# Optimization experiments

Hardware: AMD Instinct MI355X
Metric: run time of the kernel (lower is better)

## Reference

```python
import jax, jax.numpy as jnp
import numpy as np

B, N, D_IN, D, E, MAXD = 16, 512, 256, 64, 32, 50
LN_EPS = 1e-5

def setup_inputs() -> dict:
    key = jax.random.key(0)
    ks = jax.random.split(key, 24)
    s = lambda fan: 1.0 / np.sqrt(fan)
    inp = {
        'x': jax.random.normal(ks[0], (B, N, D_IN), jnp.float32),
        'price_rising_ranks': jax.random.randint(ks[1], (B, N), 0, N, jnp.int64),
        'Wp': jax.random.normal(ks[2], (D_IN, D), jnp.float32) * s(D_IN),
        'bp': jnp.zeros((D,), jnp.float32),
        'Wq': jax.random.normal(ks[3], (D, D), jnp.float32) * s(D),
        'bq': jnp.zeros((D,), jnp.float32),
        'Wk': jax.random.normal(ks[4], (D, D), jnp.float32) * s(D),
        'bk': jnp.zeros((D,), jnp.float32),
        'Wv': jax.random.normal(ks[5], (D, D), jnp.float32) * s(D),
        'bv': jnp.zeros((D,), jnp.float32),
        'Eemb': jax.random.normal(ks[6], (MAXD + 1, E), jnp.float32),
        'Wr1': jax.random.normal(ks[7], (E, 16), jnp.float32) * s(E),
        'br1': jnp.zeros((16,), jnp.float32),
        'Wr2': jax.random.normal(ks[8], (16, 1), jnp.float32) * s(16),
        'Wf1': jax.random.normal(ks[9], (D, 2 * D), jnp.float32) * s(D),
        'bf1': jnp.zeros((2 * D,), jnp.float32),
        'Wf2': jax.random.normal(ks[10], (2 * D, D), jnp.float32) * s(2 * D),
        'bf2': jnp.zeros((D,), jnp.float32),
        'ln_g': jnp.ones((D,), jnp.float32),
        'ln_b': jnp.zeros((D,), jnp.float32),
        'Ws1': jax.random.normal(ks[11], (D, 32), jnp.float32) * s(D),
        'bs1': jnp.zeros((32,), jnp.float32),
        'Ws2': jax.random.normal(ks[12], (32, 1), jnp.float32) * s(32),
        'bs2': jnp.zeros((1,), jnp.float32),
    }
    return inp

def reference(x, price_rising_ranks, Wp, bp, Wq, bq, Wk, bk, Wv, bv,
              Eemb, Wr1, br1, Wr2, Wf1, bf1, Wf2, bf2, ln_g, ln_b,
              Ws1, bs1, Ws2, bs2):
    xp = x @ Wp + bp                                  # (B,N,D)
    q = xp @ Wq + bq
    k = xp @ Wk + bk
    v = xp @ Wv + bv
    scores = jnp.einsum('bnd,bmd->bnm', q, k) / jnp.sqrt(jnp.float32(D))
    # rank-distance pairwise bias
    r = price_rising_ranks
    dists = jnp.clip(jnp.abs(r[:, :, None] - r[:, None, :]), 0, MAXD)  # (B,N,N) int
    emb = Eemb[dists]                                 # (B,N,N,E)
    w = jax.nn.relu(emb @ Wr1 + br1) @ Wr2            # (B,N,N,1)
    rel = jax.nn.sigmoid(w[..., 0])                   # (B,N,N)
    scores = scores * rel
    attn = jax.nn.softmax(scores, axis=-1)
    ao = jnp.einsum('bnm,bmd->bnd', attn, v)
    # feed forward + layernorm
    h = jax.nn.relu(ao @ Wf1 + bf1) @ Wf2 + bf2
    mu = jnp.mean(h, axis=-1, keepdims=True)
    var = jnp.mean((h - mu) ** 2, axis=-1, keepdims=True)
    hn = (h - mu) / jnp.sqrt(var + LN_EPS) * ln_g + ln_b
    # score projection
    out = jax.nn.relu(hn @ Ws1 + bs1) @ Ws2 + bs2     # (B,N,1)
    return jax.nn.sigmoid(out[..., 0])                # (B,N)
```

## Files before the change

kernel.cpp:

```cpp
#include <hip/hip_runtime.h>

using f32x4 = __attribute__((ext_vector_type(4))) float;
using s16x8 = __attribute__((ext_vector_type(8))) short;

static __device__ __forceinline__ unsigned short f2bf(float f){
  union { float f; unsigned int i; } c; c.f = f;
  return (unsigned short)((c.i + 0x7FFFu + ((c.i >> 16) & 1u)) >> 16);
}
static __device__ __forceinline__ s16x8 ld8(const unsigned short* p){
  return *(const s16x8*)p;
}
static __device__ __forceinline__ s16x8 cvt8(const float* p){
  const float4* q = (const float4*)p;
  float4 a = q[0], b = q[1];
  s16x8 r;
  r[0]=(short)f2bf(a.x); r[1]=(short)f2bf(a.y); r[2]=(short)f2bf(a.z); r[3]=(short)f2bf(a.w);
  r[4]=(short)f2bf(b.x); r[5]=(short)f2bf(b.y); r[6]=(short)f2bf(b.z); r[7]=(short)f2bf(b.w);
  return r;
}
static __device__ __forceinline__ f32x4 mfma16(s16x8 a, s16x8 b, f32x4 c){
  return __builtin_amdgcn_mfma_f32_16x16x32_bf16(a, b, c, 0, 0, 0);
}

__global__ __launch_bounds__(128) void k_proj(const float* __restrict__ x,
    const float* __restrict__ Wp, const float* __restrict__ bp,
    const float* __restrict__ Wq, const float* __restrict__ bq,
    const float* __restrict__ Wk, const float* __restrict__ bk,
    const float* __restrict__ Wv, const float* __restrict__ bv,
    const float* __restrict__ Ee, const float* __restrict__ Wr1,
    const float* __restrict__ br1, const float* __restrict__ Wr2,
    unsigned short* __restrict__ q, unsigned short* __restrict__ kk,
    unsigned short* __restrict__ vt, float* __restrict__ rel_t)
{
  __shared__ __align__(16) unsigned short WpT[64*264];
  __shared__ __align__(16) unsigned short Wt3[3][64*72];
  __shared__ __align__(16) unsigned short xs[2][16*72];

  int t = threadIdx.x;
  for (int i = t; i < 256*64; i += 128){
    int k = i >> 6, n = i & 63;
    WpT[n*264 + k] = f2bf(Wp[i]);
  }
  for (int i = t; i < 64*64; i += 128){
    int k2 = i >> 6, n = i & 63;
    Wt3[0][n*72 + k2] = f2bf(Wq[i]);
    Wt3[1][n*72 + k2] = f2bf(Wk[i]);
    Wt3[2][n*72 + k2] = f2bf(Wv[i]);
  }
  if (blockIdx.x == 0 && t < 51){
    float e[32];
    for (int j = 0; j < 32; ++j) e[j] = Ee[t*32 + j];
    float w = 0.f;
    for (int h = 0; h < 16; ++h){
      float s = br1[h];
      for (int j = 0; j < 32; ++j) s += e[j] * Wr1[j*16 + h];
      w += fmaxf(s, 0.f) * Wr2[h];
    }
    rel_t[t] = 1.f / (1.f + __expf(-w));
  }
  __syncthreads();

  int lane = t & 63, wave = t >> 6, colL = lane & 15, quad = lane >> 4;
  int row0 = blockIdx.x*32 + wave*16;

  const float* xr = x + (row0 + colL)*256;
  f32x4 acc[4] = {};
  for (int kc = 0; kc < 256; kc += 32){
    s16x8 a = cvt8(xr + kc + quad*8);
#pragma unroll
    for (int nt = 0; nt < 4; ++nt)
      acc[nt] = mfma16(a, ld8(&WpT[(nt*16+colL)*264 + kc + quad*8]), acc[nt]);
  }
  unsigned short* xw = xs[wave];
#pragma unroll
  for (int nt = 0; nt < 4; ++nt){
    int col = nt*16 + colL;
    float bb = bp[col];
#pragma unroll
    for (int i = 0; i < 4; ++i)
      xw[(quad*4+i)*72 + col] = f2bf(acc[nt][i] + bb);
  }
  s16x8 a0 = ld8(&xw[colL*72 +  0 + quad*8]);
  s16x8 a1 = ld8(&xw[colL*72 + 32 + quad*8]);

#pragma unroll
  for (int w = 0; w < 3; ++w){
    const float* bias = w==0 ? bq : (w==1 ? bk : bv);
    f32x4 c[4] = {};
#pragma unroll
    for (int nt = 0; nt < 4; ++nt){
      c[nt] = mfma16(a0, ld8(&Wt3[w][(nt*16+colL)*72 +  0 + quad*8]), c[nt]);
      c[nt] = mfma16(a1, ld8(&Wt3[w][(nt*16+colL)*72 + 32 + quad*8]), c[nt]);
    }
#pragma unroll
    for (int nt = 0; nt < 4; ++nt){
      int col = nt*16 + colL;
      float bb = bias[col];
#pragma unroll
      for (int i = 0; i < 4; ++i){
        int row = row0 + quad*4 + i;
        float v = c[nt][i] + bb;
        if (w == 0)      q [row*64 + col] = f2bf(v);
        else if (w == 1) kk[row*64 + col] = f2bf(v);
        else             vt[(row>>9)*32768 + col*512 + (row & 511)] = f2bf(v);
      }
    }
  }
}

__global__ __launch_bounds__(256) void k_attn(const unsigned short* __restrict__ q,
    const unsigned short* __restrict__ kmat, const unsigned short* __restrict__ vt,
    const int* __restrict__ ranks, const float* __restrict__ rel_t,
    unsigned short* __restrict__ ao)
{
  int b = blockIdx.y, qt = blockIdx.x;
  int t = threadIdx.x, lane = t & 63, wave = t >> 6;
  int colL = lane & 15, quad = lane >> 4;

  __shared__ int r_s[512];
  __shared__ float rt_s[64];
  __shared__ __align__(16) unsigned short P[4][16*136];
  __shared__ float Opart[4][16*66];
  __shared__ float pmax_s[4][16], psum_s[4][16];

  for (int i = t; i < 512; i += 256) r_s[i] = ranks[b*512 + i];
  if (t < 64) rt_s[t] = (t < 51) ? rel_t[t] : 0.f;
  __syncthreads();

  int qrow0 = qt*16;
  const unsigned short* qp = q    + b*32768;
  const unsigned short* kp = kmat + b*32768;
  const unsigned short* vp = vt   + b*32768;

  s16x8 aq0 = ld8(qp + (qrow0+colL)*64 +  0 + quad*8);
  s16x8 aq1 = ld8(qp + (qrow0+colL)*64 + 32 + quad*8);

  int key0 = wave*128;
  f32x4 S[8];
#pragma unroll
  for (int mt = 0; mt < 8; ++mt){
    int key = key0 + mt*16 + colL;
    f32x4 c = {};
    c = mfma16(aq0, ld8(kp + key*64 +  0 + quad*8), c);
    c = mfma16(aq1, ld8(kp + key*64 + 32 + quad*8), c);
    S[mt] = c;
  }

  int rq[4];
#pragma unroll
  for (int i = 0; i < 4; ++i) rq[i] = r_s[qrow0 + quad*4 + i];

  float rmax[4] = {-1e30f,-1e30f,-1e30f,-1e30f};
#pragma unroll
  for (int mt = 0; mt < 8; ++mt){
    int rm = r_s[key0 + mt*16 + colL];
#pragma unroll
    for (int i = 0; i < 4; ++i){
      int dd = rq[i] - rm; dd = dd < 0 ? -dd : dd; dd = dd > 50 ? 50 : dd;
      float s = S[mt][i] * 0.125f * rt_s[dd];
      S[mt][i] = s;
      rmax[i] = fmaxf(rmax[i], s);
    }
  }
#pragma unroll
  for (int i = 0; i < 4; ++i){
    rmax[i] = fmaxf(rmax[i], __shfl_xor(rmax[i], 1));
    rmax[i] = fmaxf(rmax[i], __shfl_xor(rmax[i], 2));
    rmax[i] = fmaxf(rmax[i], __shfl_xor(rmax[i], 4));
    rmax[i] = fmaxf(rmax[i], __shfl_xor(rmax[i], 8));
  }
  if (colL == 0){
#pragma unroll
    for (int i = 0; i < 4; ++i) pmax_s[wave][quad*4 + i] = rmax[i];
  }
  __syncthreads();
  float gmax[4];
#pragma unroll
  for (int i = 0; i < 4; ++i){
    int r = quad*4 + i;
    gmax[i] = fmaxf(fmaxf(pmax_s[0][r], pmax_s[1][r]), fmaxf(pmax_s[2][r], pmax_s[3][r]));
  }
  float rsum[4] = {0.f,0.f,0.f,0.f};
#pragma unroll
  for (int mt = 0; mt < 8; ++mt){
#pragma unroll
    for (int i = 0; i < 4; ++i){
      float p = __expf(S[mt][i] - gmax[i]);
      S[mt][i] = p;
      rsum[i] += p;
    }
  }
#pragma unroll
  for (int i = 0; i < 4; ++i){
    rsum[i] += __shfl_xor(rsum[i], 1);
    rsum[i] += __shfl_xor(rsum[i], 2);
    rsum[i] += __shfl_xor(rsum[i], 4);
    rsum[i] += __shfl_xor(rsum[i], 8);
  }
  if (colL == 0){
#pragma unroll
    for (int i = 0; i < 4; ++i) psum_s[wave][quad*4 + i] = rsum[i];
  }
  __syncthreads();
  float inv[4];
#pragma unroll
  for (int i = 0; i < 4; ++i){
    int r = quad*4 + i;
    inv[i] = 1.f / (psum_s[0][r] + psum_s[1][r] + psum_s[2][r] + psum_s[3][r]);
  }
  unsigned short* Pw = P[wave];
#pragma unroll
  for (int mt = 0; mt < 8; ++mt){
#pragma unroll
    for (int i = 0; i < 4; ++i)
      Pw[(quad*4+i)*136 + mt*16 + colL] = f2bf(S[mt][i] * inv[i]);
  }
  f32x4 O[4] = {};
#pragma unroll
  for (int mc = 0; mc < 128; mc += 32){
    s16x8 ap = ld8(&Pw[colL*136 + mc + quad*8]);
#pragma unroll
    for (int dt = 0; dt < 4; ++dt)
      O[dt] = mfma16(ap, ld8(vp + (dt*16+colL)*512 + key0 + mc + quad*8), O[dt]);
  }
  float* Ow = Opart[wave];
#pragma unroll
  for (int dt = 0; dt < 4; ++dt)
#pragma unroll
    for (int i = 0; i < 4; ++i)
      Ow[(quad*4+i)*66 + dt*16 + colL] = O[dt][i];
  __syncthreads();
  for (int e = t; e < 1024; e += 256){
    int row = e >> 6, col = e & 63;
    float s = Opart[0][row*66+col] + Opart[1][row*66+col]
            + Opart[2][row*66+col] + Opart[3][row*66+col];
    ao[(b*512 + qrow0 + row)*64 + col] = f2bf(s);
  }
}

__global__ __launch_bounds__(128) void k_ffn(const unsigned short* __restrict__ ao,
    const float* __restrict__ Wf1, const float* __restrict__ bf1,
    const float* __restrict__ Wf2, const float* __restrict__ bf2,
    const float* __restrict__ lng, const float* __restrict__ lnb,
    const float* __restrict__ Ws1, const float* __restrict__ bs1,
    const float* __restrict__ Ws2, const float* __restrict__ bs2,
    float* __restrict__ out)
{
  __shared__ __align__(16) unsigned short Wf1t[128*72];
  __shared__ __align__(16) unsigned short Wf2t[64*136];
  __shared__ __align__(16) unsigned short Ws1t[32*72];
  __shared__ __align__(16) unsigned short hbuf[2][16*136];
  __shared__ float cb[384];

  int t = threadIdx.x;
  for (int i = t; i < 64*128; i += 128){ int d = i>>7, j = i&127; Wf1t[j*72 + d] = f2bf(Wf1[i]); }
  for (int i = t; i < 128*64; i += 128){ int kx = i>>6, n = i&63; Wf2t[n*136 + kx] = f2bf(Wf2[i]); }
  for (int i = t; i < 64*32;  i += 128){ int d = i>>5, c = i&31; Ws1t[c*72 + d] = f2bf(Ws1[i]); }
  if (t < 128) cb[t] = bf1[t];
  if (t < 64){ cb[128+t] = bf2[t]; cb[192+t] = lng[t]; cb[256+t] = lnb[t]; }
  if (t < 32){ cb[320+t] = bs1[t]; cb[352+t] = Ws2[t]; }
  __syncthreads();

  int lane = t & 63, wave = t >> 6, colL = lane & 15, quad = lane >> 4;
  int row0 = blockIdx.x*32 + wave*16;
  unsigned short* hw = hbuf[wave];

  f32x4 a1[8] = {};
#pragma unroll
  for (int kc = 0; kc < 64; kc += 32){
    s16x8 a = ld8(ao + (row0+colL)*64 + kc + quad*8);
#pragma unroll
    for (int nt = 0; nt < 8; ++nt)
      a1[nt] = mfma16(a, ld8(&Wf1t[(nt*16+colL)*72 + kc + quad*8]), a1[nt]);
  }
#pragma unroll
  for (int nt = 0; nt < 8; ++nt){
    int col = nt*16 + colL;
    float bb = cb[col];
#pragma unroll
    for (int i = 0; i < 4; ++i)
      hw[(quad*4+i)*136 + col] = f2bf(fmaxf(a1[nt][i] + bb, 0.f));
  }
  f32x4 a2[4] = {};
#pragma unroll
  for (int kc = 0; kc < 128; kc += 32){
    s16x8 a = ld8(&hw[colL*136 + kc + quad*8]);
#pragma unroll
    for (int nt = 0; nt < 4; ++nt)
      a2[nt] = mfma16(a, ld8(&Wf2t[(nt*16+colL)*136 + kc + quad*8]), a2[nt]);
  }
  float vals[4][4];
#pragma unroll
  for (int nt = 0; nt < 4; ++nt){
    float bb = cb[128 + nt*16 + colL];
#pragma unroll
    for (int i = 0; i < 4; ++i) vals[i][nt] = a2[nt][i] + bb;
  }
  float hnv[4][4];
#pragma unroll
  for (int i = 0; i < 4; ++i){
    float s = vals[i][0]+vals[i][1]+vals[i][2]+vals[i][3];
    s += __shfl_xor(s,1); s += __shfl_xor(s,2); s += __shfl_xor(s,4); s += __shfl_xor(s,8);
    float mu = s * (1.f/64.f);
    float d0=vals[i][0]-mu, d1=vals[i][1]-mu, d2=vals[i][2]-mu, d3=vals[i][3]-mu;
    float s2 = d0*d0 + d1*d1 + d2*d2 + d3*d3;
    s2 += __shfl_xor(s2,1); s2 += __shfl_xor(s2,2); s2 += __shfl_xor(s2,4); s2 += __shfl_xor(s2,8);
    float invs = rsqrtf(s2*(1.f/64.f) + 1e-5f);
#pragma unroll
    for (int nt = 0; nt < 4; ++nt){
      int col = nt*16 + colL;
      hnv[i][nt] = (vals[i][nt]-mu)*invs*cb[192+col] + cb[256+col];
    }
  }
#pragma unroll
  for (int i = 0; i < 4; ++i)
#pragma unroll
    for (int nt = 0; nt < 4; ++nt)
      hw[(quad*4+i)*72 + nt*16 + colL] = f2bf(hnv[i][nt]);

  f32x4 a3[2] = {};
#pragma unroll
  for (int kc = 0; kc < 64; kc += 32){
    s16x8 a = ld8(&hw[colL*72 + kc + quad*8]);
#pragma unroll
    for (int nt = 0; nt < 2; ++nt)
      a3[nt] = mfma16(a, ld8(&Ws1t[(nt*16+colL)*72 + kc + quad*8]), a3[nt]);
  }
  float bs2f = bs2[0];
#pragma unroll
  for (int i = 0; i < 4; ++i){
    float p = 0.f;
#pragma unroll
    for (int nt = 0; nt < 2; ++nt){
      int col = nt*16 + colL;
      p += fmaxf(a3[nt][i] + cb[320+col], 0.f) * cb[352+col];
    }
    p += __shfl_xor(p,1); p += __shfl_xor(p,2); p += __shfl_xor(p,4); p += __shfl_xor(p,8);
    if (colL == 0){
      float z = p + bs2f;
      out[row0 + quad*4 + i] = 1.f / (1.f + __expf(-z));
    }
  }
}

extern "C" void kernel_launch(void* const* d_in, const int* in_sizes, int n_in,
                              void* d_out, int out_size, void* d_ws, size_t ws_size,
                              hipStream_t stream)
{
  const float* x    = (const float*)d_in[0];
  const int*   rank = (const int*)d_in[1];
  const float* Wp   = (const float*)d_in[2];
  const float* bp   = (const float*)d_in[3];
  const float* Wq   = (const float*)d_in[4];
  const float* bq   = (const float*)d_in[5];
  const float* Wk   = (const float*)d_in[6];
  const float* bk   = (const float*)d_in[7];
  const float* Wv   = (const float*)d_in[8];
  const float* bv   = (const float*)d_in[9];
  const float* Ee   = (const float*)d_in[10];
  const float* Wr1  = (const float*)d_in[11];
  const float* br1  = (const float*)d_in[12];
  const float* Wr2  = (const float*)d_in[13];
  const float* Wf1  = (const float*)d_in[14];
  const float* bf1  = (const float*)d_in[15];
  const float* Wf2  = (const float*)d_in[16];
  const float* bf2  = (const float*)d_in[17];
  const float* lng  = (const float*)d_in[18];
  const float* lnb  = (const float*)d_in[19];
  const float* Ws1  = (const float*)d_in[20];
  const float* bs1  = (const float*)d_in[21];
  const float* Ws2  = (const float*)d_in[22];
  const float* bs2  = (const float*)d_in[23];
  float* out = (float*)d_out;

  char* ws = (char*)d_ws;
  float*          rel_t = (float*)(ws + 0);
  unsigned short* q     = (unsigned short*)(ws + 256);
  unsigned short* kk    = (unsigned short*)(ws + 256 + 1*1048576);
  unsigned short* vt    = (unsigned short*)(ws + 256 + 2*1048576);
  unsigned short* ao    = (unsigned short*)(ws + 256 + 3*1048576);

  k_proj<<<dim3(256), dim3(128), 0, stream>>>(x, Wp, bp, Wq, bq, Wk, bk, Wv, bv,
                                              Ee, Wr1, br1, Wr2, q, kk, vt, rel_t);
  k_attn<<<dim3(32, 16), dim3(256), 0, stream>>>(q, kk, vt, rank, rel_t, ao);
  k_ffn<<<dim3(256), dim3(128), 0, stream>>>(ao, Wf1, bf1, Wf2, bf2, lng, lnb,
                                             Ws1, bs1, Ws2, bs2, out);
}
```

Before: 146.4 us.

## Fuse projection, attention and FFN into one cooperative kernel with grid sync

Replaces the three separate launches (projection, attention, FFN) with a single cooperative kernel of 256 blocks x 512 threads. Phases are separated by a grid-wide sync, and attention output stays in LDS so the FFN runs without a global round trip for ao. The rel-bias table and FFN weight staging are built per block in parallel with the projection waves. The aim is to remove launch gaps and the ao write/read. In exchange it relies on cooperative launch residency (the old three-kernel path is kept as a fallback) and pays the cost of a grid barrier and redundant per-block weight conversion.

Result: slower. 277.7 us (+89.7%).

```diff
diff --git a/kernel.cpp b/kernel.cpp
--- a/kernel.cpp
+++ b/kernel.cpp
@@ -1,4 +1,7 @@
 #include <hip/hip_runtime.h>
+#include <hip/hip_cooperative_groups.h>
+
+namespace cg = cooperative_groups;
 
 using f32x4 = __attribute__((ext_vector_type(4))) float;
 using s16x8 = __attribute__((ext_vector_type(8))) short;
@@ -20,6 +23,325 @@
 }
 static __device__ __forceinline__ f32x4 mfma16(s16x8 a, s16x8 b, f32x4 c){
   return __builtin_amdgcn_mfma_f32_16x16x32_bf16(a, b, c, 0, 0, 0);
+}
+
+struct Params {
+  const float *x; const int *ranks;
+  const float *Wp, *bp, *Wq, *bq, *Wk, *bk, *Wv, *bv;
+  const float *Ee, *Wr1, *br1, *Wr2;
+  const float *Wf1, *bf1, *Wf2, *bf2, *lng, *lnb, *Ws1, *bs1, *Ws2, *bs2;
+  unsigned short *qg, *kg, *vg;
+  float *out;
+};
+
+__global__ __launch_bounds__(512, 2) void k_fused(Params P)
+{
+  __shared__ __align__(16) char sm[118528];
+  int*   r_s    = (int*)  sm;
+  float* rt_s   = (float*)(sm + 2048);
+  float* pmax_s = (float*)(sm + 2304);
+  float* psum_s = (float*)(sm + 2816);
+  unsigned short* aoS  = (unsigned short*)(sm + 3328);
+  unsigned short* Wf1t = (unsigned short*)(sm + 7936);
+  unsigned short* Wf2t = (unsigned short*)(sm + 26368);
+  unsigned short* Ws1t = (unsigned short*)(sm + 43776);
+  float* cb            = (float*)(sm + 48384);
+  char* scr = sm + 49920;
+  unsigned short* WpT  = (unsigned short*)scr;
+  unsigned short* Wt3  = (unsigned short*)(scr + 33792);
+  unsigned short* xs   = (unsigned short*)(scr + 61440);
+  unsigned short* Pbuf = (unsigned short*)scr;
+  float*          Opart= (float*)(scr + 34816);
+  unsigned short* hbuf = (unsigned short*)scr;
+
+  int t = threadIdx.x, bid = blockIdx.x;
+  int lane = t & 63, wave = t >> 6, colL = lane & 15, quad = lane >> 4;
+
+  for (int i = t; i < 256*64; i += 512){ int k = i >> 6, n = i & 63; WpT[n*264 + k] = f2bf(P.Wp[i]); }
+  for (int i = t; i < 64*64; i += 512){
+    int k2 = i >> 6, n = i & 63;
+    Wt3[       n*72 + k2] = f2bf(P.Wq[i]);
+    Wt3[4608 + n*72 + k2] = f2bf(P.Wk[i]);
+    Wt3[9216 + n*72 + k2] = f2bf(P.Wv[i]);
+  }
+  r_s[t] = P.ranks[(bid >> 4)*512 + t];
+  __syncthreads();
+
+  if (wave < 2){
+    int row0 = bid*32 + wave*16;
+    const float* xr = P.x + (row0 + colL)*256;
+    f32x4 acc[4] = {};
+    for (int kc = 0; kc < 256; kc += 32){
+      s16x8 a = cvt8(xr + kc + quad*8);
+#pragma unroll
+      for (int nt = 0; nt < 4; ++nt)
+        acc[nt] = mfma16(a, ld8(&WpT[(nt*16+colL)*264 + kc + quad*8]), acc[nt]);
+    }
+    unsigned short* xw = xs + wave*(16*72);
+#pragma unroll
+    for (int nt = 0; nt < 4; ++nt){
+      int col = nt*16 + colL;
+      float bb = P.bp[col];
+#pragma unroll
+      for (int i = 0; i < 4; ++i)
+        xw[(quad*4+i)*72 + col] = f2bf(acc[nt][i] + bb);
+    }
+    s16x8 a0 = ld8(&xw[colL*72 +  0 + quad*8]);
+    s16x8 a1 = ld8(&xw[colL*72 + 32 + quad*8]);
+#pragma unroll
+    for (int w = 0; w < 3; ++w){
+      const float* bias = w==0 ? P.bq : (w==1 ? P.bk : P.bv);
+      const unsigned short* Wt = Wt3 + w*4608;
+      f32x4 c[4] = {};
+#pragma unroll
+      for (int nt = 0; nt < 4; ++nt){
+        c[nt] = mfma16(a0, ld8(&Wt[(nt*16+colL)*72 +  0 + quad*8]), c[nt]);
+        c[nt] = mfma16(a1, ld8(&Wt[(nt*16+colL)*72 + 32 + quad*8]), c[nt]);
+      }
+#pragma unroll
+      for (int nt = 0; nt < 4; ++nt){
+        int col = nt*16 + colL;
+        float bb = bias[col];
+#pragma unroll
+        for (int i = 0; i < 4; ++i){
+          int row = row0 + quad*4 + i;
+          float v = c[nt][i] + bb;
+          if (w == 0)      P.qg[row*64 + col] = f2bf(v);
+          else if (w == 1) P.kg[row*64 + col] = f2bf(v);
+          else             P.vg[(row>>9)*32768 + col*512 + (row & 511)] = f2bf(v);
+        }
+      }
+    }
+  } else if (wave == 7){
+    int dd = t - 448;
+    if (dd < 51){
+      float e[32];
+#pragma unroll
+      for (int j = 0; j < 32; ++j) e[j] = P.Ee[dd*32 + j];
+      float w = 0.f;
+      for (int h = 0; h < 16; ++h){
+        float s = P.br1[h];
+#pragma unroll
+        for (int j = 0; j < 32; ++j) s += e[j] * P.Wr1[j*16 + h];
+        w += fmaxf(s, 0.f) * P.Wr2[h];
+      }
+      rt_s[dd] = 1.f / (1.f + __expf(-w));
+    } else {
+      rt_s[dd] = 0.f;
+    }
+  } else {
+    int u = t - 128;
+    for (int i = u; i < 64*128; i += 320){ int d = i>>7, j = i&127; Wf1t[j*72 + d] = f2bf(P.Wf1[i]); }
+    for (int i = u; i < 128*64; i += 320){ int kx = i>>6, n = i&63; Wf2t[n*136 + kx] = f2bf(P.Wf2[i]); }
+    for (int i = u; i < 64*32;  i += 320){ int d = i>>5, c = i&31; Ws1t[c*72 + d] = f2bf(P.Ws1[i]); }
+    if (u < 128) cb[u] = P.bf1[u];
+    if (u < 64){ cb[128+u] = P.bf2[u]; cb[192+u] = P.lng[u]; cb[256+u] = P.lnb[u]; }
+    if (u < 32){ cb[320+u] = P.bs1[u]; cb[352+u] = P.Ws2[u]; }
+  }
+
+  __threadfence();
+  cg::this_grid().sync();
+  __threadfence();
+
+  int group = wave >> 2, kw = wave & 3;
+  {
+    int l = bid*2 + group;
+    int b = l >> 5, qt = l & 31;
+    int qrow0 = qt*16;
+    const unsigned short* qp = P.qg + b*32768;
+    const unsigned short* kp = P.kg + b*32768;
+    const unsigned short* vp = P.vg + b*32768;
+
+    s16x8 aq0 = ld8(qp + (qrow0+colL)*64 +  0 + quad*8);
+    s16x8 aq1 = ld8(qp + (qrow0+colL)*64 + 32 + quad*8);
+
+    int key0 = kw*128;
+    f32x4 Sv[8];
+#pragma unroll
+    for (int mt = 0; mt < 8; ++mt){
+      int key = key0 + mt*16 + colL;
+      f32x4 c = {};
+      c = mfma16(aq0, ld8(kp + key*64 +  0 + quad*8), c);
+      c = mfma16(aq1, ld8(kp + key*64 + 32 + quad*8), c);
+      Sv[mt] = c;
+    }
+
+    int rq[4];
+#pragma unroll
+    for (int i = 0; i < 4; ++i) rq[i] = r_s[qrow0 + quad*4 + i];
+
+    float rmax[4] = {-1e30f,-1e30f,-1e30f,-1e30f};
+#pragma unroll
+    for (int mt = 0; mt < 8; ++mt){
+      int rm = r_s[key0 + mt*16 + colL];
+#pragma unroll
+      for (int i = 0; i < 4; ++i){
+        int dd = rq[i] - rm; dd = dd < 0 ? -dd : dd; dd = dd > 50 ? 50 : dd;
+        float s = Sv[mt][i] * 0.125f * rt_s[dd];
+        Sv[mt][i] = s;
+        rmax[i] = fmaxf(rmax[i], s);
+      }
+    }
+#pragma unroll
+    for (int i = 0; i < 4; ++i){
+      rmax[i] = fmaxf(rmax[i], __shfl_xor(rmax[i], 1));
+      rmax[i] = fmaxf(rmax[i], __shfl_xor(rmax[i], 2));
+      rmax[i] = fmaxf(rmax[i], __shfl_xor(rmax[i], 4));
+      rmax[i] = fmaxf(rmax[i], __shfl_xor(rmax[i], 8));
+    }
+    if (colL == 0){
+#pragma unroll
+      for (int i = 0; i < 4; ++i) pmax_s[wave*16 + quad*4 + i] = rmax[i];
+    }
+    __syncthreads();
+    float gmax[4];
+#pragma unroll
+    for (int i = 0; i < 4; ++i){
+      int r = (group*4)*16 + quad*4 + i;
+      gmax[i] = fmaxf(fmaxf(pmax_s[r], pmax_s[r+16]), fmaxf(pmax_s[r+32], pmax_s[r+48]));
+    }
+    float rsum[4] = {0.f,0.f,0.f,0.f};
+#pragma unroll
+    for (int mt = 0; mt < 8; ++mt){
+#pragma unroll
+      for (int i = 0; i < 4; ++i){
+        float p = __expf(Sv[mt][i] - gmax[i]);
+        Sv[mt][i] = p;
+        rsum[i] += p;
+      }
+    }
+#pragma unroll
+    for (int i = 0; i < 4; ++i){
+      rsum[i] += __shfl_xor(rsum[i], 1);
+      rsum[i] += __shfl_xor(rsum[i], 2);
+      rsum[i] += __shfl_xor(rsum[i], 4);
+      rsum[i] += __shfl_xor(rsum[i], 8);
+    }
+    if (colL == 0){
+#pragma unroll
+      for (int i = 0; i < 4; ++i) psum_s[wave*16 + quad*4 + i] = rsum[i];
+    }
+    __syncthreads();
+    float inv[4];
+#pragma unroll
+    for (int i = 0; i < 4; ++i){
+      int r = (group*4)*16 + quad*4 + i;
+      inv[i] = 1.f / (psum_s[r] + psum_s[r+16] + psum_s[r+32] + psum_s[r+48]);
+    }
+    unsigned short* Pw = Pbuf + wave*(16*136);
+#pragma unroll
+    for (int mt = 0; mt < 8; ++mt){
+#pragma unroll
+      for (int i = 0; i < 4; ++i)
+        Pw[(quad*4+i)*136 + mt*16 + colL] = f2bf(Sv[mt][i] * inv[i]);
+    }
+    f32x4 O[4] = {};
+#pragma unroll
+    for (int mc = 0; mc < 128; mc += 32){
+      s16x8 ap = ld8(&Pw[colL*136 + mc + quad*8]);
+#pragma unroll
+      for (int dt = 0; dt < 4; ++dt)
+        O[dt] = mfma16(ap, ld8(vp + (dt*16+colL)*512 + key0 + mc + quad*8), O[dt]);
+    }
+    float* Ow = Opart + wave*(16*66);
+#pragma unroll
+    for (int dt = 0; dt < 4; ++dt)
+#pragma unroll
+      for (int i = 0; i < 4; ++i)
+        Ow[(quad*4+i)*66 + dt*16 + colL] = O[dt][i];
+    __syncthreads();
+    int tg = t & 255;
+    const float* Og = Opart + (group*4)*(16*66);
+    for (int e = tg; e < 1024; e += 256){
+      int row = e >> 6, col = e & 63;
+      float s = Og[row*66+col] + Og[1056 + row*66+col]
+              + Og[2112 + row*66+col] + Og[3168 + row*66+col];
+      aoS[(group*16 + row)*72 + col] = f2bf(s);
+    }
+  }
+  __syncthreads();
+
+  if (wave < 2){
+    unsigned short* hw = hbuf + wave*(16*136);
+    int row0 = bid*32 + wave*16;
+
+    f32x4 a1[8] = {};
+#pragma unroll
+    for (int kc = 0; kc < 64; kc += 32){
+      s16x8 a = ld8(&aoS[(wave*16 + colL)*72 + kc + quad*8]);
+#pragma unroll
+      for (int nt = 0; nt < 8; ++nt)
+        a1[nt] = mfma16(a, ld8(&Wf1t[(nt*16+colL)*72 + kc + quad*8]), a1[nt]);
+    }
+#pragma unroll
+    for (int nt = 0; nt < 8; ++nt){
+      int col = nt*16 + colL;
+      float bb = cb[col];
+#pragma unroll
+      for (int i = 0; i < 4; ++i)
+        hw[(quad*4+i)*136 + col] = f2bf(fmaxf(a1[nt][i] + bb, 0.f));
+    }
+    f32x4 a2[4] = {};
+#pragma unroll
+    for (int kc = 0; kc < 128; kc += 32){
+      s16x8 a = ld8(&hw[colL*136 + kc + quad*8]);
+#pragma unroll
+      for (int nt = 0; nt < 4; ++nt)
+        a2[nt] = mfma16(a, ld8(&Wf2t[(nt*16+colL)*136 + kc + quad*8]), a2[nt]);
+    }
+    float vals[4][4];
+#pragma unroll
+    for (int nt = 0; nt < 4; ++nt){
+      float bb = cb[128 + nt*16 + colL];
+#pragma unroll
+      for (int i = 0; i < 4; ++i) vals[i][nt] = a2[nt][i] + bb;
+    }
+    float hnv[4][4];
+#pragma unroll
+    for (int i = 0; i < 4; ++i){
+      float s = vals[i][0]+vals[i][1]+vals[i][2]+vals[i][3];
+      s += __shfl_xor(s,1); s += __shfl_xor(s,2); s += __shfl_xor(s,4); s += __shfl_xor(s,8);
+      float mu = s * (1.f/64.f);
+      float d0=vals[i][0]-mu, d1=vals[i][1]-mu, d2=vals[i][2]-mu, d3=vals[i][3]-mu;
+      float s2 = d0*d0 + d1*d1 + d2*d2 + d3*d3;
+      s2 += __shfl_xor(s2,1); s2 += __shfl_xor(s2,2); s2 += __shfl_xor(s2,4); s2 += __shfl_xor(s2,8);
+      float invs = rsqrtf(s2*(1.f/64.f) + 1e-5f);
+#pragma unroll
+      for (int nt = 0; nt < 4; ++nt){
+        int col = nt*16 + colL;
+        hnv[i][nt] = (vals[i][nt]-mu)*invs*cb[192+col] + cb[256+col];
+      }
+    }
+#pragma unroll
+    for (int i = 0; i < 4; ++i)
+#pragma unroll
+      for (int nt = 0; nt < 4; ++nt)
+        hw[(quad*4+i)*72 + nt*16 + colL] = f2bf(hnv[i][nt]);
+
+    f32x4 a3[2] = {};
+#pragma unroll
+    for (int kc = 0; kc < 64; kc += 32){
+      s16x8 a = ld8(&hw[colL*72 + kc + quad*8]);
+#pragma unroll
+      for (int nt = 0; nt < 2; ++nt)
+        a3[nt] = mfma16(a, ld8(&Ws1t[(nt*16+colL)*72 + kc + quad*8]), a3[nt]);
+    }
+    float bs2f = P.bs2[0];
+#pragma unroll
+    for (int i = 0; i < 4; ++i){
+      float p = 0.f;
+#pragma unroll
+      for (int nt = 0; nt < 2; ++nt){
+        int col = nt*16 + colL;
+        p += fmaxf(a3[nt][i] + cb[320+col], 0.f) * cb[352+col];
+      }
+      p += __shfl_xor(p,1); p += __shfl_xor(p,2); p += __shfl_xor(p,4); p += __shfl_xor(p,8);
+      if (colL == 0){
+        float z = p + bs2f;
+        P.out[row0 + quad*4 + i] = 1.f / (1.f + __expf(-z));
+      }
+    }
+  }
 }
 
 __global__ __launch_bounds__(128) void k_proj(const float* __restrict__ x,
@@ -119,7 +441,7 @@
 
   __shared__ int r_s[512];
   __shared__ float rt_s[64];
-  __shared__ __align__(16) unsigned short P[4][16*136];
+  __shared__ __align__(16) unsigned short Pl[4][16*136];
   __shared__ float Opart[4][16*66];
   __shared__ float pmax_s[4][16], psum_s[4][16];
 
@@ -208,7 +530,7 @@
     int r = quad*4 + i;
     inv[i] = 1.f / (psum_s[0][r] + psum_s[1][r] + psum_s[2][r] + psum_s[3][r]);
   }
-  unsigned short* Pw = P[wave];
+  unsigned short* Pw = Pl[wave];
 #pragma unroll
   for (int mt = 0; mt < 8; ++mt){
 #pragma unroll
@@ -380,9 +702,18 @@
   unsigned short* vt    = (unsigned short*)(ws + 256 + 2*1048576);
   unsigned short* ao    = (unsigned short*)(ws + 256 + 3*1048576);
 
-  k_proj<<<dim3(256), dim3(128), 0, stream>>>(x, Wp, bp, Wq, bq, Wk, bk, Wv, bv,
-                                              Ee, Wr1, br1, Wr2, q, kk, vt, rel_t);
-  k_attn<<<dim3(32, 16), dim3(256), 0, stream>>>(q, kk, vt, rank, rel_t, ao);
-  k_ffn<<<dim3(256), dim3(128), 0, stream>>>(ao, Wf1, bf1, Wf2, bf2, lng, lnb,
-                                             Ws1, bs1, Ws2, bs2, out);
-}
+  Params p{ x, rank, Wp, bp, Wq, bq, Wk, bk, Wv, bv,
+            Ee, Wr1, br1, Wr2,
+            Wf1, bf1, Wf2, bf2, lng, lnb, Ws1, bs1, Ws2, bs2,
+            q, kk, vt, out };
+  void* args[] = { (void*)&p };
+  hipError_t err = hipLaunchCooperativeKernel(k_fused, dim3(256), dim3(512),
+                                              args, 0u, stream);
+  if (err != hipSuccess){
+    k_proj<<<dim3(256), dim3(128), 0, stream>>>(x, Wp, bp, Wq, bq, Wk, bk, Wv, bv,
+                                                Ee, Wr1, br1, Wr2, q, kk, vt, rel_t);
+    k_attn<<<dim3(32, 16), dim3(256), 0, stream>>>(q, kk, vt, rank, rel_t, ao);
+    k_ffn<<<dim3(256), dim3(128), 0, stream>>>(ao, Wf1, bf1, Wf2, bf2, lng, lnb,
+                                               Ws1, bs1, Ws2, bs2, out);
+  }
+}
```

## Fuse attention and FFN kernels, vectorize weight staging, prefetch x in projection

Applied to the files above, without the earlier changes.

The attention and feed-forward/LayerNorm/score stages are merged into one kernel, so the attention output stays in shared memory and the separate FFN launch plus its global round trip are removed. Each fused block now converts the FFN weights to bf16 on its own, which means 512 blocks repeat that conversion instead of 256, and only one wave runs the FFN tail. Weight loads in both kernels use float4 reads. k_proj adds a third wave that touches x early to warm the cache and computes the relation table, which runs alongside the weight staging.

After: 136.1 us. 1.08x faster.

```diff
diff --git a/kernel.cpp b/kernel.cpp
--- a/kernel.cpp
+++ b/kernel.cpp
@@ -22,7 +22,7 @@
   return __builtin_amdgcn_mfma_f32_16x16x32_bf16(a, b, c, 0, 0, 0);
 }
 
-__global__ __launch_bounds__(128) void k_proj(const float* __restrict__ x,
+__global__ __launch_bounds__(192) void k_proj(const float* __restrict__ x,
     const float* __restrict__ Wp, const float* __restrict__ bp,
     const float* __restrict__ Wq, const float* __restrict__ bq,
     const float* __restrict__ Wk, const float* __restrict__ bk,
@@ -37,208 +37,108 @@
   __shared__ __align__(16) unsigned short xs[2][16*72];
 
   int t = threadIdx.x;
-  for (int i = t; i < 256*64; i += 128){
-    int k = i >> 6, n = i & 63;
-    WpT[n*264 + k] = f2bf(Wp[i]);
-  }
-  for (int i = t; i < 64*64; i += 128){
-    int k2 = i >> 6, n = i & 63;
-    Wt3[0][n*72 + k2] = f2bf(Wq[i]);
-    Wt3[1][n*72 + k2] = f2bf(Wk[i]);
-    Wt3[2][n*72 + k2] = f2bf(Wv[i]);
-  }
-  if (blockIdx.x == 0 && t < 51){
+  int row0b = blockIdx.x*32;
+
+  const float4* xb4 = (const float4*)(x + row0b*256);
+  float4 tc0 = xb4[((t*2  ) & 255)*8];
+  float4 tc1 = xb4[((t*2+1) & 255)*8];
+
+  const float4* Wp4 = (const float4*)Wp;
+  for (int i = t; i < 4096; i += 192){
+    float4 v = Wp4[i];
+    int k = i >> 4, n = (i & 15) * 4;
+    WpT[(n+0)*264+k] = f2bf(v.x);
+    WpT[(n+1)*264+k] = f2bf(v.y);
+    WpT[(n+2)*264+k] = f2bf(v.z);
+    WpT[(n+3)*264+k] = f2bf(v.w);
+  }
+  const float4* Wq4 = (const float4*)Wq;
+  const float4* Wk4 = (const float4*)Wk;
+  const float4* Wv4 = (const float4*)Wv;
+  for (int i = t; i < 1024; i += 192){
+    int k = i >> 4, n = (i & 15) * 4;
+    float4 a = Wq4[i], b2 = Wk4[i], c2 = Wv4[i];
+    Wt3[0][(n+0)*72+k]=f2bf(a.x);  Wt3[0][(n+1)*72+k]=f2bf(a.y);
+    Wt3[0][(n+2)*72+k]=f2bf(a.z);  Wt3[0][(n+3)*72+k]=f2bf(a.w);
+    Wt3[1][(n+0)*72+k]=f2bf(b2.x); Wt3[1][(n+1)*72+k]=f2bf(b2.y);
+    Wt3[1][(n+2)*72+k]=f2bf(b2.z); Wt3[1][(n+3)*72+k]=f2bf(b2.w);
+    Wt3[2][(n+0)*72+k]=f2bf(c2.x); Wt3[2][(n+1)*72+k]=f2bf(c2.y);
+    Wt3[2][(n+2)*72+k]=f2bf(c2.z); Wt3[2][(n+3)*72+k]=f2bf(c2.w);
+  }
+  if (blockIdx.x == 0 && t >= 128 && t < 179){
+    int dd = t - 128;
     float e[32];
-    for (int j = 0; j < 32; ++j) e[j] = Ee[t*32 + j];
+    const float4* e4 = (const float4*)(Ee + dd*32);
+#pragma unroll
+    for (int j = 0; j < 8; ++j){
+      float4 v = e4[j];
+      e[j*4+0]=v.x; e[j*4+1]=v.y; e[j*4+2]=v.z; e[j*4+3]=v.w;
+    }
     float w = 0.f;
     for (int h = 0; h < 16; ++h){
       float s = br1[h];
+#pragma unroll
       for (int j = 0; j < 32; ++j) s += e[j] * Wr1[j*16 + h];
       w += fmaxf(s, 0.f) * Wr2[h];
     }
-    rel_t[t] = 1.f / (1.f + __expf(-w));
-  }
-  __syncthreads();
-
-  int lane = t & 63, wave = t >> 6, colL = lane & 15, quad = lane >> 4;
-  int row0 = blockIdx.x*32 + wave*16;
-
-  const float* xr = x + (row0 + colL)*256;
-  f32x4 acc[4] = {};
-  for (int kc = 0; kc < 256; kc += 32){
-    s16x8 a = cvt8(xr + kc + quad*8);
-#pragma unroll
-    for (int nt = 0; nt < 4; ++nt)
-      acc[nt] = mfma16(a, ld8(&WpT[(nt*16+colL)*264 + kc + quad*8]), acc[nt]);
-  }
-  unsigned short* xw = xs[wave];
-#pragma unroll
-  for (int nt = 0; nt < 4; ++nt){
-    int col = nt*16 + colL;
-    float bb = bp[col];
-#pragma unroll
-    for (int i = 0; i < 4; ++i)
-      xw[(quad*4+i)*72 + col] = f2bf(acc[nt][i] + bb);
-  }
-  s16x8 a0 = ld8(&xw[colL*72 +  0 + quad*8]);
-  s16x8 a1 = ld8(&xw[colL*72 + 32 + quad*8]);
-
-#pragma unroll
-  for (int w = 0; w < 3; ++w){
-    const float* bias = w==0 ? bq : (w==1 ? bk : bv);
-    f32x4 c[4] = {};
-#pragma unroll
-    for (int nt = 0; nt < 4; ++nt){
-      c[nt] = mfma16(a0, ld8(&Wt3[w][(nt*16+colL)*72 +  0 + quad*8]), c[nt]);
-      c[nt] = mfma16(a1, ld8(&Wt3[w][(nt*16+colL)*72 + 32 + quad*8]), c[nt]);
-    }
+    rel_t[dd] = 1.f / (1.f + __expf(-w));
+  }
+  asm volatile("" :: "v"(tc0.x), "v"(tc1.x));
+  __syncthreads();
+
+  if (t < 128){
+    int lane = t & 63, wave = t >> 6, colL = lane & 15, quad = lane >> 4;
+    int row0 = row0b + wave*16;
+
+    const float* xr = x + (row0 + colL)*256;
+    f32x4 acc[4] = {};
+    for (int kc = 0; kc < 256; kc += 32){
+      s16x8 a = cvt8(xr + kc + quad*8);
+#pragma unroll
+      for (int nt = 0; nt < 4; ++nt)
+        acc[nt] = mfma16(a, ld8(&WpT[(nt*16+colL)*264 + kc + quad*8]), acc[nt]);
+    }
+    unsigned short* xw = xs[wave];
 #pragma unroll
     for (int nt = 0; nt < 4; ++nt){
       int col = nt*16 + colL;
-      float bb = bias[col];
-#pragma unroll
-      for (int i = 0; i < 4; ++i){
-        int row = row0 + quad*4 + i;
-        float v = c[nt][i] + bb;
-        if (w == 0)      q [row*64 + col] = f2bf(v);
-        else if (w == 1) kk[row*64 + col] = f2bf(v);
-        else             vt[(row>>9)*32768 + col*512 + (row & 511)] = f2bf(v);
+      float bb = bp[col];
+#pragma unroll
+      for (int i = 0; i < 4; ++i)
+        xw[(quad*4+i)*72 + col] = f2bf(acc[nt][i] + bb);
+    }
+    s16x8 a0 = ld8(&xw[colL*72 +  0 + quad*8]);
+    s16x8 a1 = ld8(&xw[colL*72 + 32 + quad*8]);
+
+#pragma unroll
+    for (int w = 0; w < 3; ++w){
+      const float* bias = w==0 ? bq : (w==1 ? bk : bv);
+      f32x4 c[4] = {};
+#pragma unroll
+      for (int nt = 0; nt < 4; ++nt){
+        c[nt] = mfma16(a0, ld8(&Wt3[w][(nt*16+colL)*72 +  0 + quad*8]), c[nt]);
+        c[nt] = mfma16(a1, ld8(&Wt3[w][(nt*16+colL)*72 + 32 + quad*8]), c[nt]);
       }
-    }
-  }
-}
-
-__global__ __launch_bounds__(256) void k_attn(const unsigned short* __restrict__ q,
+#pragma unroll
+      for (int nt = 0; nt < 4; ++nt){
+        int col = nt*16 + colL;
+        float bb = bias[col];
+#pragma unroll
+        for (int i = 0; i < 4; ++i){
+          int row = row0 + quad*4 + i;
+          float v = c[nt][i] + bb;
+          if (w == 0)      q [row*64 + col] = f2bf(v);
+          else if (w == 1) kk[row*64 + col] = f2bf(v);
+          else             vt[(row>>9)*32768 + col*512 + (row & 511)] = f2bf(v);
+        }
+      }
+    }
+  }
+}
+
+__global__ __launch_bounds__(256) void k_attn_ffn(const unsigned short* __restrict__ q,
     const unsigned short* __restrict__ kmat, const unsigned short* __restrict__ vt,
     const int* __restrict__ ranks, const float* __restrict__ rel_t,
-    unsigned short* __restrict__ ao)
-{
-  int b = blockIdx.y, qt = blockIdx.x;
-  int t = threadIdx.x, lane = t & 63, wave = t >> 6;
-  int colL = lane & 15, quad = lane >> 4;
-
-  __shared__ int r_s[512];
-  __shared__ float rt_s[64];
-  __shared__ __align__(16) unsigned short P[4][16*136];
-  __shared__ float Opart[4][16*66];
-  __shared__ float pmax_s[4][16], psum_s[4][16];
-
-  for (int i = t; i < 512; i += 256) r_s[i] = ranks[b*512 + i];
-  if (t < 64) rt_s[t] = (t < 51) ? rel_t[t] : 0.f;
-  __syncthreads();
-
-  int qrow0 = qt*16;
-  const unsigned short* qp = q    + b*32768;
-  const unsigned short* kp = kmat + b*32768;
-  const unsigned short* vp = vt   + b*32768;
-
-  s16x8 aq0 = ld8(qp + (qrow0+colL)*64 +  0 + quad*8);
-  s16x8 aq1 = ld8(qp + (qrow0+colL)*64 + 32 + quad*8);
-
-  int key0 = wave*128;
-  f32x4 S[8];
-#pragma unroll
-  for (int mt = 0; mt < 8; ++mt){
-    int key = key0 + mt*16 + colL;
-    f32x4 c = {};
-    c = mfma16(aq0, ld8(kp + key*64 +  0 + quad*8), c);
-    c = mfma16(aq1, ld8(kp + key*64 + 32 + quad*8), c);
-    S[mt] = c;
-  }
-
-  int rq[4];
-#pragma unroll
-  for (int i = 0; i < 4; ++i) rq[i] = r_s[qrow0 + quad*4 + i];
-
-  float rmax[4] = {-1e30f,-1e30f,-1e30f,-1e30f};
-#pragma unroll
-  for (int mt = 0; mt < 8; ++mt){
-    int rm = r_s[key0 + mt*16 + colL];
-#pragma unroll
-    for (int i = 0; i < 4; ++i){
-      int dd = rq[i] - rm; dd = dd < 0 ? -dd : dd; dd = dd > 50 ? 50 : dd;
-      float s = S[mt][i] * 0.125f * rt_s[dd];
-      S[mt][i] = s;
-      rmax[i] = fmaxf(rmax[i], s);
-    }
-  }
-#pragma unroll
-  for (int i = 0; i < 4; ++i){
-    rmax[i] = fmaxf(rmax[i], __shfl_xor(rmax[i], 1));
-    rmax[i] = fmaxf(rmax[i], __shfl_xor(rmax[i], 2));
-    rmax[i] = fmaxf(rmax[i], __shfl_xor(rmax[i], 4));
-    rmax[i] = fmaxf(rmax[i], __shfl_xor(rmax[i], 8));
-  }
-  if (colL == 0){
-#pragma unroll
-    for (int i = 0; i < 4; ++i) pmax_s[wave][quad*4 + i] = rmax[i];
-  }
-  __syncthreads();
-  float gmax[4];
-#pragma unroll
-  for (int i = 0; i < 4; ++i){
-    int r = quad*4 + i;
-    gmax[i] = fmaxf(fmaxf(pmax_s[0][r], pmax_s[1][r]), fmaxf(pmax_s[2][r], pmax_s[3][r]));
-  }
-  float rsum[4] = {0.f,0.f,0.f,0.f};
-#pragma unroll
-  for (int mt = 0; mt < 8; ++mt){
-#pragma unroll
-    for (int i = 0; i < 4; ++i){
-      float p = __expf(S[mt][i] - gmax[i]);
-      S[mt][i] = p;
-      rsum[i] += p;
-    }
-  }
-#pragma unroll
-  for (int i = 0; i < 4; ++i){
-    rsum[i] += __shfl_xor(rsum[i], 1);
-    rsum[i] += __shfl_xor(rsum[i], 2);
-    rsum[i] += __shfl_xor(rsum[i], 4);
-    rsum[i] += __shfl_xor(rsum[i], 8);
-  }
-  if (colL == 0){
-#pragma unroll
-    for (int i = 0; i < 4; ++i) psum_s[wave][quad*4 + i] = rsum[i];
-  }
-  __syncthreads();
-  float inv[4];
-#pragma unroll
-  for (int i = 0; i < 4; ++i){
-    int r = quad*4 + i;
-    inv[i] = 1.f / (psum_s[0][r] + psum_s[1][r] + psum_s[2][r] + psum_s[3][r]);
-  }
-  unsigned short* Pw = P[wave];
-#pragma unroll
-  for (int mt = 0; mt < 8; ++mt){
-#pragma unroll
-    for (int i = 0; i < 4; ++i)
-      Pw[(quad*4+i)*136 + mt*16 + colL] = f2bf(S[mt][i] * inv[i]);
-  }
-  f32x4 O[4] = {};
-#pragma unroll
-  for (int mc = 0; mc < 128; mc += 32){
-    s16x8 ap = ld8(&Pw[colL*136 + mc + quad*8]);
-#pragma unroll
-    for (int dt = 0; dt < 4; ++dt)
-      O[dt] = mfma16(ap, ld8(vp + (dt*16+colL)*512 + key0 + mc + quad*8), O[dt]);
-  }
-  float* Ow = Opart[wave];
-#pragma unroll
-  for (int dt = 0; dt < 4; ++dt)
-#pragma unroll
-    for (int i = 0; i < 4; ++i)
-      Ow[(quad*4+i)*66 + dt*16 + colL] = O[dt][i];
-  __syncthreads();
-  for (int e = t; e < 1024; e += 256){
-    int row = e >> 6, col = e & 63;
-    float s = Opart[0][row*66+col] + Opart[1][row*66+col]
-            + Opart[2][row*66+col] + Opart[3][row*66+col];
-    ao[(b*512 + qrow0 + row)*64 + col] = f2bf(s);
-  }
-}
-
-__global__ __launch_bounds__(128) void k_ffn(const unsigned short* __restrict__ ao,
     const float* __restrict__ Wf1, const float* __restrict__ bf1,
     const float* __restrict__ Wf2, const float* __restrict__ bf2,
     const float* __restrict__ lng, const float* __restrict__ lnb,
@@ -246,99 +146,239 @@
     const float* __restrict__ Ws2, const float* __restrict__ bs2,
     float* __restrict__ out)
 {
+  __shared__ __align__(16) int r_s[512];
+  __shared__ float rt_s[64];
+  __shared__ float pmax_s[4][16], psum_s[4][16];
+  __shared__ __align__(16) unsigned short Pbuf[4*16*136];
+  __shared__ __align__(16) float Opart[4][16*66];
   __shared__ __align__(16) unsigned short Wf1t[128*72];
   __shared__ __align__(16) unsigned short Wf2t[64*136];
   __shared__ __align__(16) unsigned short Ws1t[32*72];
-  __shared__ __align__(16) unsigned short hbuf[2][16*136];
   __shared__ float cb[384];
 
-  int t = threadIdx.x;
-  for (int i = t; i < 64*128; i += 128){ int d = i>>7, j = i&127; Wf1t[j*72 + d] = f2bf(Wf1[i]); }
-  for (int i = t; i < 128*64; i += 128){ int kx = i>>6, n = i&63; Wf2t[n*136 + kx] = f2bf(Wf2[i]); }
-  for (int i = t; i < 64*32;  i += 128){ int d = i>>5, c = i&31; Ws1t[c*72 + d] = f2bf(Ws1[i]); }
+  int b = blockIdx.y, qt = blockIdx.x;
+  int t = threadIdx.x, lane = t & 63, wave = t >> 6;
+  int colL = lane & 15, quad = lane >> 4;
+
+  if (t < 128) ((int4*)r_s)[t] = ((const int4*)(ranks + b*512))[t];
+  if (t < 64) rt_s[t] = (t < 51) ? rel_t[t] : 0.f;
+  const float4* Wf14 = (const float4*)Wf1;
+  for (int i = t; i < 2048; i += 256){
+    float4 v = Wf14[i];
+    int d = i >> 5, j = (i & 31) * 4;
+    Wf1t[(j+0)*72+d]=f2bf(v.x); Wf1t[(j+1)*72+d]=f2bf(v.y);
+    Wf1t[(j+2)*72+d]=f2bf(v.z); Wf1t[(j+3)*72+d]=f2bf(v.w);
+  }
+  const float4* Wf24 = (const float4*)Wf2;
+  for (int i = t; i < 2048; i += 256){
+    float4 v = Wf24[i];
+    int kx = i >> 4, n = (i & 15) * 4;
+    Wf2t[(n+0)*136+kx]=f2bf(v.x); Wf2t[(n+1)*136+kx]=f2bf(v.y);
+    Wf2t[(n+2)*136+kx]=f2bf(v.z); Wf2t[(n+3)*136+kx]=f2bf(v.w);
+  }
+  const float4* Ws14 = (const float4*)Ws1;
+  for (int i = t; i < 512; i += 256){
+    float4 v = Ws14[i];
+    int d = i >> 3, c0 = (i & 7) * 4;
+    Ws1t[(c0+0)*72+d]=f2bf(v.x); Ws1t[(c0+1)*72+d]=f2bf(v.y);
+    Ws1t[(c0+2)*72+d]=f2bf(v.z); Ws1t[(c0+3)*72+d]=f2bf(v.w);
+  }
   if (t < 128) cb[t] = bf1[t];
   if (t < 64){ cb[128+t] = bf2[t]; cb[192+t] = lng[t]; cb[256+t] = lnb[t]; }
   if (t < 32){ cb[320+t] = bs1[t]; cb[352+t] = Ws2[t]; }
-  __syncthreads();
-
-  int lane = t & 63, wave = t >> 6, colL = lane & 15, quad = lane >> 4;
-  int row0 = blockIdx.x*32 + wave*16;
-  unsigned short* hw = hbuf[wave];
-
-  f32x4 a1[8] = {};
-#pragma unroll
-  for (int kc = 0; kc < 64; kc += 32){
-    s16x8 a = ld8(ao + (row0+colL)*64 + kc + quad*8);
-#pragma unroll
-    for (int nt = 0; nt < 8; ++nt)
-      a1[nt] = mfma16(a, ld8(&Wf1t[(nt*16+colL)*72 + kc + quad*8]), a1[nt]);
-  }
-#pragma unroll
-  for (int nt = 0; nt < 8; ++nt){
-    int col = nt*16 + colL;
-    float bb = cb[col];
+
+  int qrow0 = qt*16;
+  const unsigned short* qp = q    + b*32768;
+  const unsigned short* kp = kmat + b*32768;
+  const unsigned short* vp = vt   + b*32768;
+
+  s16x8 aq0 = ld8(qp + (qrow0+colL)*64 +  0 + quad*8);
+  s16x8 aq1 = ld8(qp + (qrow0+colL)*64 + 32 + quad*8);
+
+  int key0 = wave*128;
+  f32x4 S[8];
+#pragma unroll
+  for (int mt = 0; mt < 8; ++mt){
+    int key = key0 + mt*16 + colL;
+    f32x4 c = {};
+    c = mfma16(aq0, ld8(kp + key*64 +  0 + quad*8), c);
+    c = mfma16(aq1, ld8(kp + key*64 + 32 + quad*8), c);
+    S[mt] = c;
+  }
+  __syncthreads();
+
+  int rq[4];
+#pragma unroll
+  for (int i = 0; i < 4; ++i) rq[i] = r_s[qrow0 + quad*4 + i];
+
+  float rmax[4] = {-1e30f,-1e30f,-1e30f,-1e30f};
+#pragma unroll
+  for (int mt = 0; mt < 8; ++mt){
+    int rm = r_s[key0 + mt*16 + colL];
+#pragma unroll
+    for (int i = 0; i < 4; ++i){
+      int dd = rq[i] - rm; dd = dd < 0 ? -dd : dd; dd = dd > 50 ? 50 : dd;
+      float s = S[mt][i] * 0.125f * rt_s[dd];
+      S[mt][i] = s;
+      rmax[i] = fmaxf(rmax[i], s);
+    }
+  }
+#pragma unroll
+  for (int i = 0; i < 4; ++i){
+    rmax[i] = fmaxf(rmax[i], __shfl_xor(rmax[i], 1));
+    rmax[i] = fmaxf(rmax[i], __shfl_xor(rmax[i], 2));
+    rmax[i] = fmaxf(rmax[i], __shfl_xor(rmax[i], 4));
+    rmax[i] = fmaxf(rmax[i], __shfl_xor(rmax[i], 8));
+  }
+  if (colL == 0){
+#pragma unroll
+    for (int i = 0; i < 4; ++i) pmax_s[wave][quad*4 + i] = rmax[i];
+  }
+  __syncthreads();
+  float gmax[4];
+#pragma unroll
+  for (int i = 0; i < 4; ++i){
+    int r = quad*4 + i;
+    gmax[i] = fmaxf(fmaxf(pmax_s[0][r], pmax_s[1][r]), fmaxf(pmax_s[2][r], pmax_s[3][r]));
+  }
+  float rsum[4] = {0.f,0.f,0.f,0.f};
+#pragma unroll
+  for (int mt = 0; mt < 8; ++mt){
+#pragma unroll
+    for (int i = 0; i < 4; ++i){
+      float p = __expf(S[mt][i] - gmax[i]);
+      S[mt][i] = p;
+      rsum[i] += p;
+    }
+  }
+#pragma unroll
+  for (int i = 0; i < 4; ++i){
+    rsum[i] += __shfl_xor(rsum[i], 1);
+    rsum[i] += __shfl_xor(rsum[i], 2);
+    rsum[i] += __shfl_xor(rsum[i], 4);
+    rsum[i] += __shfl_xor(rsum[i], 8);
+  }
+  if (colL == 0){
+#pragma unroll
+    for (int i = 0; i < 4; ++i) psum_s[wave][quad*4 + i] = rsum[i];
+  }
+  __syncthreads();
+  float inv[4];
+#pragma unroll
+  for (int i = 0; i < 4; ++i){
+    int r = quad*4 + i;
+    inv[i] = 1.f / (psum_s[0][r] + psum_s[1][r] + psum_s[2][r] + psum_s[3][r]);
+  }
+  unsigned short* Pw = Pbuf + wave*(16*136);
+#pragma unroll
+  for (int mt = 0; mt < 8; ++mt){
 #pragma unroll
     for (int i = 0; i < 4; ++i)
-      hw[(quad*4+i)*136 + col] = f2bf(fmaxf(a1[nt][i] + bb, 0.f));
-  }
-  f32x4 a2[4] = {};
-#pragma unroll
-  for (int kc = 0; kc < 128; kc += 32){
-    s16x8 a = ld8(&hw[colL*136 + kc + quad*8]);
-#pragma unroll
-    for (int nt = 0; nt < 4; ++nt)
-      a2[nt] = mfma16(a, ld8(&Wf2t[(nt*16+colL)*136 + kc + quad*8]), a2[nt]);
-  }
-  float vals[4][4];
-#pragma unroll
-  for (int nt = 0; nt < 4; ++nt){
-    float bb = cb[128 + nt*16 + colL];
-#pragma unroll
-    for (int i = 0; i < 4; ++i) vals[i][nt] = a2[nt][i] + bb;
-  }
-  float hnv[4][4];
-#pragma unroll
-  for (int i = 0; i < 4; ++i){
-    float s = vals[i][0]+vals[i][1]+vals[i][2]+vals[i][3];
-    s += __shfl_xor(s,1); s += __shfl_xor(s,2); s += __shfl_xor(s,4); s += __shfl_xor(s,8);
-    float mu = s * (1.f/64.f);
-    float d0=vals[i][0]-mu, d1=vals[i][1]-mu, d2=vals[i][2]-mu, d3=vals[i][3]-mu;
-    float s2 = d0*d0 + d1*d1 + d2*d2 + d3*d3;
-    s2 += __shfl_xor(s2,1); s2 += __shfl_xor(s2,2); s2 += __shfl_xor(s2,4); s2 += __shfl_xor(s2,8);
-    float invs = rsqrtf(s2*(1.f/64.f) + 1e-5f);
+      Pw[(quad*4+i)*136 + mt*16 + colL] = f2bf(S[mt][i] * inv[i]);
+  }
+  f32x4 O[4] = {};
+#pragma unroll
+  for (int mc = 0; mc < 128; mc += 32){
+    s16x8 ap = ld8(&Pw[colL*136 + mc + quad*8]);
+#pragma unroll
+    for (int dt = 0; dt < 4; ++dt)
+      O[dt] = mfma16(ap, ld8(vp + (dt*16+colL)*512 + key0 + mc + quad*8), O[dt]);
+  }
+  float* Ow = Opart[wave];
+#pragma unroll
+  for (int dt = 0; dt < 4; ++dt)
+#pragma unroll
+    for (int i = 0; i < 4; ++i)
+      Ow[(quad*4+i)*66 + dt*16 + colL] = O[dt][i];
+  __syncthreads();
+  unsigned short* aoS = Pbuf;
+  for (int e = t; e < 1024; e += 256){
+    int row = e >> 6, col = e & 63;
+    float s = Opart[0][row*66+col] + Opart[1][row*66+col]
+            + Opart[2][row*66+col] + Opart[3][row*66+col];
+    aoS[row*72 + col] = f2bf(s);
+  }
+  __syncthreads();
+
+  if (wave == 0){
+    unsigned short* hw = Pbuf + 2176;
+    int row0g = b*512 + qt*16;
+
+    f32x4 a1[8] = {};
+#pragma unroll
+    for (int kc = 0; kc < 64; kc += 32){
+      s16x8 a = ld8(&aoS[colL*72 + kc + quad*8]);
+#pragma unroll
+      for (int nt = 0; nt < 8; ++nt)
+        a1[nt] = mfma16(a, ld8(&Wf1t[(nt*16+colL)*72 + kc + quad*8]), a1[nt]);
+    }
+#pragma unroll
+    for (int nt = 0; nt < 8; ++nt){
+      int col = nt*16 + colL;
+      float bb = cb[col];
+#pragma unroll
+      for (int i = 0; i < 4; ++i)
+        hw[(quad*4+i)*136 + col] = f2bf(fmaxf(a1[nt][i] + bb, 0.f));
+    }
+    f32x4 a2[4] = {};
+#pragma unroll
+    for (int kc = 0; kc < 128; kc += 32){
+      s16x8 a = ld8(&hw[colL*136 + kc + quad*8]);
+#pragma unroll
+      for (int nt = 0; nt < 4; ++nt)
+        a2[nt] = mfma16(a, ld8(&Wf2t[(nt*16+colL)*136 + kc + quad*8]), a2[nt]);
+    }
+    float vals[4][4];
 #pragma unroll
     for (int nt = 0; nt < 4; ++nt){
-      int col = nt*16 + colL;
-      hnv[i][nt] = (vals[i][nt]-mu)*invs*cb[192+col] + cb[256+col];
-    }
-  }
-#pragma unroll
-  for (int i = 0; i < 4; ++i)
-#pragma unroll
-    for (int nt = 0; nt < 4; ++nt)
-      hw[(quad*4+i)*72 + nt*16 + colL] = f2bf(hnv[i][nt]);
-
-  f32x4 a3[2] = {};
-#pragma unroll
-  for (int kc = 0; kc < 64; kc += 32){
-    s16x8 a = ld8(&hw[colL*72 + kc + quad*8]);
-#pragma unroll
-    for (int nt = 0; nt < 2; ++nt)
-      a3[nt] = mfma16(a, ld8(&Ws1t[(nt*16+colL)*72 + kc + quad*8]), a3[nt]);
-  }
-  float bs2f = bs2[0];
-#pragma unroll
-  for (int i = 0; i < 4; ++i){
-    float p = 0.f;
-#pragma unroll
-    for (int nt = 0; nt < 2; ++nt){
-      int col = nt*16 + colL;
-      p += fmaxf(a3[nt][i] + cb[320+col], 0.f) * cb[352+col];
-    }
-    p += __shfl_xor(p,1); p += __shfl_xor(p,2); p += __shfl_xor(p,4); p += __shfl_xor(p,8);
-    if (colL == 0){
-      float z = p + bs2f;
-      out[row0 + quad*4 + i] = 1.f / (1.f + __expf(-z));
+      float bb = cb[128 + nt*16 + colL];
+#pragma unroll
+      for (int i = 0; i < 4; ++i) vals[i][nt] = a2[nt][i] + bb;
+    }
+    float hnv[4][4];
+#pragma unroll
+    for (int i = 0; i < 4; ++i){
+      float s = vals[i][0]+vals[i][1]+vals[i][2]+vals[i][3];
+      s += __shfl_xor(s,1); s += __shfl_xor(s,2); s += __shfl_xor(s,4); s += __shfl_xor(s,8);
+      float mu = s * (1.f/64.f);
+      float d0=vals[i][0]-mu, d1=vals[i][1]-mu, d2=vals[i][2]-mu, d3=vals[i][3]-mu;
+      float s2 = d0*d0 + d1*d1 + d2*d2 + d3*d3;
+      s2 += __shfl_xor(s2,1); s2 += __shfl_xor(s2,2); s2 += __shfl_xor(s2,4); s2 += __shfl_xor(s2,8);
+      float invs = rsqrtf(s2*(1.f/64.f) + 1e-5f);
+#pragma unroll
+      for (int nt = 0; nt < 4; ++nt){
+        int col = nt*16 + colL;
+        hnv[i][nt] = (vals[i][nt]-mu)*invs*cb[192+col] + cb[256+col];
+      }
+    }
+#pragma unroll
+    for (int i = 0; i < 4; ++i)
+#pragma unroll
+      for (int nt = 0; nt < 4; ++nt)
+        hw[(quad*4+i)*72 + nt*16 + colL] = f2bf(hnv[i][nt]);
+
+    f32x4 a3[2] = {};
+#pragma unroll
+    for (int kc = 0; kc < 64; kc += 32){
+      s16x8 a = ld8(&hw[colL*72 + kc + quad*8]);
+#pragma unroll
+      for (int nt = 0; nt < 2; ++nt)
+        a3[nt] = mfma16(a, ld8(&Ws1t[(nt*16+colL)*72 + kc + quad*8]), a3[nt]);
+    }
+    float bs2f = bs2[0];
+#pragma unroll
+    for (int i = 0; i < 4; ++i){
+      float p = 0.f;
+#pragma unroll
+      for (int nt = 0; nt < 2; ++nt){
+        int col = nt*16 + colL;
+        p += fmaxf(a3[nt][i] + cb[320+col], 0.f) * cb[352+col];
+      }
+      p += __shfl_xor(p,1); p += __shfl_xor(p,2); p += __shfl_xor(p,4); p += __shfl_xor(p,8);
+      if (colL == 0){
+        float z = p + bs2f;
+        out[row0g + quad*4 + i] = 1.f / (1.f + __expf(-z));
+      }
     }
   }
 }
@@ -378,11 +418,10 @@
   unsigned short* q     = (unsigned short*)(ws + 256);
   unsigned short* kk    = (unsigned short*)(ws + 256 + 1*1048576);
   unsigned short* vt    = (unsigned short*)(ws + 256 + 2*1048576);
-  unsigned short* ao    = (unsigned short*)(ws + 256 + 3*1048576);
-
-  k_proj<<<dim3(256), dim3(128), 0, stream>>>(x, Wp, bp, Wq, bq, Wk, bk, Wv, bv,
+
+  k_proj<<<dim3(256), dim3(192), 0, stream>>>(x, Wp, bp, Wq, bq, Wk, bk, Wv, bv,
                                               Ee, Wr1, br1, Wr2, q, kk, vt, rel_t);
-  k_attn<<<dim3(32, 16), dim3(256), 0, stream>>>(q, kk, vt, rank, rel_t, ao);
-  k_ffn<<<dim3(256), dim3(128), 0, stream>>>(ao, Wf1, bf1, Wf2, bf2, lng, lnb,
-                                             Ws1, bs1, Ws2, bs2, out);
-}
+  k_attn_ffn<<<dim3(32, 16), dim3(256), 0, stream>>>(q, kk, vt, rank, rel_t,
+                                              Wf1, bf1, Wf2, bf2, lng, lnb,
+                                              Ws1, bs1, Ws2, bs2, out);
+}
```
